# Performance work log

Hardware: AMD Instinct MI355X
Metric: run time of the kernel (lower is better)

## Reference

```python
import jax, jax.numpy as jnp
import numpy as np

EXP = 1          # module init arg `exp`
NEG = -1e9       # masked_fill value


def setup_inputs() -> dict:
    key = jax.random.key(0)
    k1, k2 = jax.random.split(key)
    lhs = jax.random.normal(k1, (8, 1023, 768), dtype=jnp.float32)
    rhs = jax.random.normal(k2, (8, 8192, 768), dtype=jnp.float32)
    return {"lhs": lhs, "rhs": rhs}


def reference(lhs, rhs):
    # lhs: [B, N_1, dim], rhs: [B, N_, dim], N = N_1 + 1, F = N_ // N
    B, N1, d = lhs.shape
    N = N1 + 1
    Ntot = rhs.shape[1]
    F = Ntot // N

    # L2-normalize along feature dim (normalize_vector)
    ln = lhs / jnp.linalg.norm(lhs, axis=-1, keepdims=True)
    rn = rhs / jnp.linalg.norm(rhs, axis=-1, keepdims=True)

    # cosine similarity: [B, N_1, N_]
    sim = jnp.einsum('bnd,bmd->bnm', ln, rn) ** EXP

    # Diagonal-window mask on the [B, N_1, F, N] view:
    #  - column 0 of each N-block -> NEG
    #  - last N_1 columns (indices 1..N_1) -> NEG except where col-1 == row
    keep = jnp.concatenate(
        [jnp.zeros((N1, 1), dtype=bool), jnp.eye(N1, dtype=bool)], axis=-1
    )  # [N_1, N]
    sim4 = sim.reshape(B, N1, F, N)
    sim4 = jnp.where(keep[None, :, None, :], sim4, NEG)
    return sim4.reshape(B, N1, Ntot)
```

## Files before the change

### kernel.cpp

```cpp
#include <hip/hip_runtime.h>

constexpr int B    = 8;
constexpr int N1   = 1023;
constexpr int NBLK = 1024;
constexpr int D    = 768;
constexpr int F    = 8;
constexpr int NTOT = 8192;
constexpr float NEG = -1e9f;

__global__ __launch_bounds__(256)
void lcs_kernel(const float* __restrict__ lhs,
                const float* __restrict__ rhs,
                float* __restrict__ out) {
    int flat = blockIdx.x;
    int f = flat % F;
    int n = (flat / F) % N1;
    int b = flat / (F * N1);

    int t = threadIdx.x;

    const float4* l4 = (const float4*)(lhs + ((size_t)b * N1 + n) * D);
    const float4* r4 = (const float4*)(rhs + ((size_t)b * NTOT + (size_t)f * NBLK + (n + 1)) * D);

    float dot = 0.f, l2 = 0.f, r2 = 0.f;
    if (t < D / 4) {
        float4 a = l4[t];
        float4 c = r4[t];
        dot = a.x * c.x + a.y * c.y + a.z * c.z + a.w * c.w;
        l2  = a.x * a.x + a.y * a.y + a.z * a.z + a.w * a.w;
        r2  = c.x * c.x + c.y * c.y + c.z * c.z + c.w * c.w;
    }

    #pragma unroll
    for (int off = 32; off >= 1; off >>= 1) {
        dot += __shfl_xor(dot, off, 64);
        l2  += __shfl_xor(l2,  off, 64);
        r2  += __shfl_xor(r2,  off, 64);
    }
    __shared__ float sdot[4], sl2[4], sr2[4];
    int wave = t >> 6;
    if ((t & 63) == 0) { sdot[wave] = dot; sl2[wave] = l2; sr2[wave] = r2; }
    __syncthreads();
    float dsum = sdot[0] + sdot[1] + sdot[2] + sdot[3];
    float lsum = sl2[0]  + sl2[1]  + sl2[2]  + sl2[3];
    float rsum = sr2[0]  + sr2[1]  + sr2[2]  + sr2[3];
    float sim = dsum * rsqrtf(lsum * rsum);

    float4* o4 = (float4*)(out + ((size_t)b * N1 + n) * NTOT + (size_t)f * NBLK);
    int keep_col = n + 1;
    int c0 = t * 4;
    float4 v;
    v.x = (c0 + 0 == keep_col) ? sim : NEG;
    v.y = (c0 + 1 == keep_col) ? sim : NEG;
    v.z = (c0 + 2 == keep_col) ? sim : NEG;
    v.w = (c0 + 3 == keep_col) ? sim : NEG;
    o4[t] = v;
}

extern "C" void kernel_launch(void* const* d_in, const int* in_sizes, int n_in,
                              void* d_out, int out_size, void* d_ws, size_t ws_size,
                              hipStream_t stream) {
    const float* lhs = (const float*)d_in[0];
    const float* rhs = (const float*)d_in[1];
    float* out = (float*)d_out;

    int grid = B * N1 * F;
    lcs_kernel<<<grid, 256, 0, stream>>>(lhs, rhs, out);
}
```

Measured before the change: 99.01 us.

## Map one wave per output row segment, issue NEG stores early with nontemporal hints

Each wave now handles one (b,n,f) segment instead of a whole 256-thread block, which removes the LDS reduction and __syncthreads. The NEG fill stores are issued before the input loads so writes overlap the reads, and nontemporal load/store builtins are meant to keep streaming traffic from polluting cache. The grid shrinks by four, and each lane now does three float4 loads and four stores. The output is write-dominated (about 268 MB), so the gain depends mostly on store efficiency.

```diff
diff --git a/kernel.cpp b/kernel.cpp
--- a/kernel.cpp
+++ b/kernel.cpp
@@ -8,28 +8,55 @@
 constexpr int NTOT = 8192;
 constexpr float NEG = -1e9f;
 
+typedef float v4f __attribute__((ext_vector_type(4)));
+
 __global__ __launch_bounds__(256)
 void lcs_kernel(const float* __restrict__ lhs,
                 const float* __restrict__ rhs,
                 float* __restrict__ out) {
-    int flat = blockIdx.x;
-    int f = flat % F;
-    int n = (flat / F) % N1;
-    int b = flat / (F * N1);
+    int t    = threadIdx.x;
+    int wave = t >> 6;
+    int lane = t & 63;
+    int gi   = blockIdx.x * 4 + wave;
 
-    int t = threadIdx.x;
+    int n   = gi % N1;
+    int tmp = gi / N1;
+    int f   = tmp % F;
+    int b   = tmp / F;
 
-    const float4* l4 = (const float4*)(lhs + ((size_t)b * N1 + n) * D);
-    const float4* r4 = (const float4*)(rhs + ((size_t)b * NTOT + (size_t)f * NBLK + (n + 1)) * D);
+    const v4f* l4 = (const v4f*)(lhs + ((size_t)b * N1 + n) * D);
+    const v4f* r4 = (const v4f*)(rhs + ((size_t)b * NTOT + (size_t)f * NBLK + (n + 1)) * D);
+    v4f*       o4 = (v4f*)(out + ((size_t)b * N1 + n) * NTOT + (size_t)f * NBLK);
 
-    float dot = 0.f, l2 = 0.f, r2 = 0.f;
-    if (t < D / 4) {
-        float4 a = l4[t];
-        float4 c = r4[t];
-        dot = a.x * c.x + a.y * c.y + a.z * c.z + a.w * c.w;
-        l2  = a.x * a.x + a.y * a.y + a.z * a.z + a.w * a.w;
-        r2  = c.x * c.x + c.y * c.y + c.z * c.z + c.w * c.w;
+    int keep_col   = n + 1;
+    int keep_q     = keep_col >> 2;
+    int owner_lane = keep_q & 63;
+    int owner_it   = keep_q >> 6;
+
+    v4f neg4 = {NEG, NEG, NEG, NEG};
+    #pragma unroll
+    for (int it = 0; it < 4; ++it) {
+        if (!(lane == owner_lane && it == owner_it)) {
+            __builtin_nontemporal_store(neg4, &o4[it * 64 + lane]);
+        }
     }
+
+    v4f a0 = l4[lane];
+    v4f a1 = l4[lane + 64];
+    v4f a2 = l4[lane + 128];
+    v4f c0 = __builtin_nontemporal_load(&r4[lane]);
+    v4f c1 = __builtin_nontemporal_load(&r4[lane + 64]);
+    v4f c2 = __builtin_nontemporal_load(&r4[lane + 128]);
+
+    float dot = a0.x*c0.x + a0.y*c0.y + a0.z*c0.z + a0.w*c0.w
+              + a1.x*c1.x + a1.y*c1.y + a1.z*c1.z + a1.w*c1.w
+              + a2.x*c2.x + a2.y*c2.y + a2.z*c2.z + a2.w*c2.w;
+    float l2  = a0.x*a0.x + a0.y*a0.y + a0.z*a0.z + a0.w*a0.w
+              + a1.x*a1.x + a1.y*a1.y + a1.z*a1.z + a1.w*a1.w
+              + a2.x*a2.x + a2.y*a2.y + a2.z*a2.z + a2.w*a2.w;
+    float r2  = c0.x*c0.x + c0.y*c0.y + c0.z*c0.z + c0.w*c0.w
+              + c1.x*c1.x + c1.y*c1.y + c1.z*c1.z + c1.w*c1.w
+              + c2.x*c2.x + c2.y*c2.y + c2.z*c2.z + c2.w*c2.w;
 
     #pragma unroll
     for (int off = 32; off >= 1; off >>= 1) {
@@ -37,24 +64,17 @@
         l2  += __shfl_xor(l2,  off, 64);
         r2  += __shfl_xor(r2,  off, 64);
     }
-    __shared__ float sdot[4], sl2[4], sr2[4];
-    int wave = t >> 6;
-    if ((t & 63) == 0) { sdot[wave] = dot; sl2[wave] = l2; sr2[wave] = r2; }
-    __syncthreads();
-    float dsum = sdot[0] + sdot[1] + sdot[2] + sdot[3];
-    float lsum = sl2[0]  + sl2[1]  + sl2[2]  + sl2[3];
-    float rsum = sr2[0]  + sr2[1]  + sr2[2]  + sr2[3];
-    float sim = dsum * rsqrtf(lsum * rsum);
+    float sim = dot * rsqrtf(l2 * r2);
 
-    float4* o4 = (float4*)(out + ((size_t)b * N1 + n) * NTOT + (size_t)f * NBLK);
-    int keep_col = n + 1;
-    int c0 = t * 4;
-    float4 v;
-    v.x = (c0 + 0 == keep_col) ? sim : NEG;
-    v.y = (c0 + 1 == keep_col) ? sim : NEG;
-    v.z = (c0 + 2 == keep_col) ? sim : NEG;
-    v.w = (c0 + 3 == keep_col) ? sim : NEG;
-    o4[t] = v;
+    if (lane == owner_lane) {
+        int r = keep_col & 3;
+        v4f v;
+        v.x = (r == 0) ? sim : NEG;
+        v.y = (r == 1) ? sim : NEG;
+        v.z = (r == 2) ? sim : NEG;
+        v.w = (r == 3) ? sim : NEG;
+        __builtin_nontemporal_store(v, &o4[owner_it * 64 + owner_lane]);
+    }
 }
 
 extern "C" void kernel_launch(void* const* d_in, const int* in_sizes, int n_in,
@@ -64,6 +84,6 @@
     const float* rhs = (const float*)d_in[1];
     float* out = (float*)d_out;
 
-    int grid = B * N1 * F;
+    int grid = (B * N1 * F) / 4;
     lcs_kernel<<<grid, 256, 0, stream>>>(lhs, rhs, out);
 }
```

Result: faster. 88.47 us (-10.6%).
